# Optimization experiments

Measured on AMD Instinct MI355X. Metric: run time of the kernel, lower is better.

The kernel has to match this reference:

```python
import jax, jax.numpy as jnp
import numpy as np

N_NODES = 50000
N_EDGES = 800000
D_IN = 128
D_OUT = 128  # hidden_size == output_size == 128


def setup_inputs() -> dict:
    key = jax.random.key(0)
    k_x, k_src, k_dst, k_w1, k_w2 = jax.random.split(key, 5)
    x = jax.random.normal(k_x, (N_NODES, D_IN), dtype=jnp.float32)
    src = jax.random.randint(k_src, (N_EDGES,), 0, N_NODES)
    dst = jax.random.randint(k_dst, (N_EDGES,), 0, N_NODES)
    # SGConv fc weight (torch Linear layout: [out, in]) and bias
    w_conv = jax.random.normal(k_w1, (D_OUT, D_IN), dtype=jnp.float32) / np.sqrt(D_IN)
    b_conv = jnp.zeros((D_OUT,), dtype=jnp.float32)
    # trailing Linear(hidden_size=128 -> output_size=128)
    w_lin = jax.random.normal(k_w2, (D_OUT, D_OUT), dtype=jnp.float32) / np.sqrt(D_OUT)
    b_lin = jnp.zeros((D_OUT,), dtype=jnp.float32)
    return {"x": x, "src": src, "dst": dst,
            "w_conv": w_conv, "b_conv": b_conv,
            "w_lin": w_lin, "b_lin": b_lin}


def reference(x, src, dst, w_conv, b_conv, w_lin, b_lin):
    n = x.shape[0]
    # symmetric normalization by in-degree (DGL SGConv, k=1 hop)
    deg = jax.ops.segment_sum(jnp.ones_like(dst, dtype=x.dtype), dst, num_segments=n)
    norm = jax.lax.rsqrt(jnp.clip(deg, 1.0))[:, None]  # [N,1]
    h = x * norm                                        # D^{-1/2} X
    h = jax.ops.segment_sum(h[src], dst, num_segments=n)  # A (D^{-1/2} X), spmm via gather+scatter-add
    h = h * norm                                        # D^{-1/2} A D^{-1/2} X
    h = jnp.maximum(h @ w_conv.T + b_conv, 0.0)         # SGConv fc + relu
    return jnp.maximum(h @ w_lin.T + b_lin, 0.0)        # Linear + relu
```

## Files before the change

### kernel.cpp

```cpp
#include <hip/hip_runtime.h>

#define N_NODES 50000
#define N_EDGES 800000
#define D 128
#define ROWS 16
#define BCAP 255
#define LCAP 64
#define EDGE_BLOCKS 782
#define XCONV_BLOCKS 3125
#define NORM_BLOCKS 196
#define WSPLIT_BLOCKS 128
#define XB_OFF 200064
#define WS_NEEDED 13000064ull

typedef int   v4i __attribute__((ext_vector_type(4)));
typedef float v4f __attribute__((ext_vector_type(4)));


__device__ __forceinline__ unsigned short bf_rne(float v) {
    unsigned u = __float_as_uint(v);
    u += 0x7FFFu + ((u >> 16) & 1u);
    return (unsigned short)(u >> 16);
}
__device__ __forceinline__ float bf_up(unsigned short h) {
    return __uint_as_float((unsigned)h << 16);
}
__device__ __forceinline__ void split_pack(float a, float b, unsigned& hw, unsigned& lw) {
    unsigned short ha = bf_rne(a);
    unsigned short hb = bf_rne(b);
    unsigned short la = bf_rne(a - bf_up(ha));
    unsigned short lb = bf_rne(b - bf_up(hb));
    hw = (unsigned)ha | ((unsigned)hb << 16);
    lw = (unsigned)la | ((unsigned)lb << 16);
}
__device__ __forceinline__ unsigned pack2(float a, float b) {
    return (unsigned)bf_rne(a) | ((unsigned)bf_rne(b) << 16);
}

__global__ void scatter_kernel(const int4* __restrict__ src4,
                               const int4* __restrict__ dst4,
                               int* __restrict__ deg,
                               unsigned short* outSlots,
                               const float* __restrict__ x,
                               unsigned short* __restrict__ xb) {
    int b = blockIdx.x, t = threadIdx.x;
    if (b < EDGE_BLOCKS) {
        int e = b * 256 + t;
        if (e < N_EDGES / 4) {
            int4 s = src4[e];
            int4 d = dst4[e];
            int p;
            p = atomicAdd(&deg[d.x], 1); if (p < BCAP) outSlots[(size_t)d.x * 256 + p] = (unsigned short)s.x;
            p = atomicAdd(&deg[d.y], 1); if (p < BCAP) outSlots[(size_t)d.y * 256 + p] = (unsigned short)s.y;
            p = atomicAdd(&deg[d.z], 1); if (p < BCAP) outSlots[(size_t)d.z * 256 + p] = (unsigned short)s.z;
            p = atomicAdd(&deg[d.w], 1); if (p < BCAP) outSlots[(size_t)d.w * 256 + p] = (unsigned short)s.w;
        }
    } else {
        int i = (b - EDGE_BLOCKS) * 256 + t;
        if (i < N_NODES * D / 8) {
            float4 a = *(const float4*)(x + (size_t)8 * i);
            float4 c = *(const float4*)(x + (size_t)8 * i + 4);
            uint4 o;
            o.x = pack2(a.x, a.y);
            o.y = pack2(a.z, a.w);
            o.z = pack2(c.x, c.y);
            o.w = pack2(c.z, c.w);
            *(uint4*)(xb + (size_t)8 * i) = o;
        }
    }
}

__global__ void prep_kernel(const int* __restrict__ deg, float* __restrict__ normArr,
                            const float* __restrict__ w1, const float* __restrict__ w2,
                            unsigned short* __restrict__ whi1, unsigned short* __restrict__ wlo1,
                            unsigned short* __restrict__ whi2, unsigned short* __restrict__ wlo2) {
    int b = blockIdx.x, t = threadIdx.x;
    if (b < NORM_BLOCKS) {
        int n = b * 256 + t;
        if (n < N_NODES)
            normArr[n] = rsqrtf(fmaxf((float)deg[n], 1.0f));
    } else {
        int m = (b - NORM_BLOCKS) * 256 + t;
        int sel = m >> 14;
        int j = m & 16383;
        float v = sel ? w2[j] : w1[j];
        unsigned short h = bf_rne(v);
        unsigned short lo = bf_rne(v - bf_up(h));
        if (sel) { whi2[j] = h; wlo2[j] = lo; }
        else     { whi1[j] = h; wlo1[j] = lo; }
    }
}

#define MLP_BODY                                                               \
    int wv = t >> 6;                                                           \
    int cb = wv << 5;                                                          \
    int l15 = l & 15;                                                          \
    int kq = l >> 4;                                                           \
    const char* phiA = (const char*)&Ahi[l15][0];                              \
    const char* ploA = (const char*)&Alo[l15][0];                              \
    v4i ahi[4], alo[4];                                                        \
_Pragma("unroll")                                                              \
    for (int kt = 0; kt < 4; ++kt) {                                           \
        int off = ((((kt << 2) | kq) ^ l15) << 4);                             \
        ahi[kt] = *(const v4i*)(phiA + off);                                   \
        alo[kt] = *(const v4i*)(ploA + off);                                   \
    }                                                                          \
    __syncthreads();                                                           \
_Pragma("unroll")                                                              \
    for (int ct = 0; ct < 2; ++ct) {                                           \
        int c = cb + (ct << 4) + l15;                                          \
        float bv = b1[c];                                                      \
        v4f acc = {bv, bv, bv, bv};                                            \
        const unsigned short* wh = whi1 + c * D + (kq << 3);                   \
        const unsigned short* wl = wlo1 + c * D + (kq << 3);                   \
_Pragma("unroll")                                                              \
        for (int kt = 0; kt < 4; ++kt) {                                       \
            v4i bh = *(const v4i*)(wh + (kt << 5));                            \
            v4i bl = *(const v4i*)(wl + (kt << 5));                            \
            asm volatile("v_mfma_f32_16x16x32_bf16 %0, %1, %2, %0" : "+v"(acc) : "v"(ahi[kt]), "v"(bh)); \
            asm volatile("v_mfma_f32_16x16x32_bf16 %0, %1, %2, %0" : "+v"(acc) : "v"(alo[kt]), "v"(bh)); \
            asm volatile("v_mfma_f32_16x16x32_bf16 %0, %1, %2, %0" : "+v"(acc) : "v"(ahi[kt]), "v"(bl)); \
        }                                                                      \
        asm volatile("s_nop 7\n\ts_nop 7" : "+v"(acc));                        \
_Pragma("unroll")                                                              \
        for (int r = 0; r < 4; ++r) {                                          \
            float v = fmaxf(acc[r], 0.0f);                                     \
            unsigned short hv = bf_rne(v);                                     \
            unsigned short lv = bf_rne(v - bf_up(hv));                         \
            int ro = (kq << 2) + r;                                            \
            int byte = (2 * c) ^ ((ro & 15) << 4);                             \
            *(unsigned short*)((char*)&Ahi[ro][0] + byte) = hv;                \
            *(unsigned short*)((char*)&Alo[ro][0] + byte) = lv;                \
        }                                                                      \
    }                                                                          \
    __syncthreads();                                                           \
_Pragma("unroll")                                                              \
    for (int kt = 0; kt < 4; ++kt) {                                           \
        int off = ((((kt << 2) | kq) ^ l15) << 4);                             \
        ahi[kt] = *(const v4i*)(phiA + off);                                   \
        alo[kt] = *(const v4i*)(ploA + off);                                   \
    }                                                                          \
_Pragma("unroll")                                                              \
    for (int ct = 0; ct < 2; ++ct) {                                           \
        int c = cb + (ct << 4) + l15;                                          \
        float bv = b2[c];                                                      \
        v4f acc = {bv, bv, bv, bv};                                            \
        const unsigned short* wh = whi2 + c * D + (kq << 3);                   \
        const unsigned short* wl = wlo2 + c * D + (kq << 3);                   \
_Pragma("unroll")                                                              \
        for (int kt = 0; kt < 4; ++kt) {                                       \
            v4i bh = *(const v4i*)(wh + (kt << 5));                            \
            v4i bl = *(const v4i*)(wl + (kt << 5));                            \
            asm volatile("v_mfma_f32_16x16x32_bf16 %0, %1, %2, %0" : "+v"(acc) : "v"(ahi[kt]), "v"(bh)); \
            asm volatile("v_mfma_f32_16x16x32_bf16 %0, %1, %2, %0" : "+v"(acc) : "v"(alo[kt]), "v"(bh)); \
            asm volatile("v_mfma_f32_16x16x32_bf16 %0, %1, %2, %0" : "+v"(acc) : "v"(ahi[kt]), "v"(bl)); \
        }                                                                      \
        asm volatile("s_nop 7\n\ts_nop 7" : "+v"(acc));                        \
_Pragma("unroll")                                                              \
        for (int r = 0; r < 4; ++r) {                                          \
            int ro = row_base + (kq << 2) + r;                                 \
            if (ro < N_NODES)                                                  \
                io[(size_t)ro * D + c] = fmaxf(acc[r], 0.0f);                  \
        }                                                                      \
    }

__global__ __launch_bounds__(256) void fused_gather_mlp_bf16(
    const unsigned short* __restrict__ xb,
    const unsigned short* slotsIn,
    const float* __restrict__ normArr, const int* __restrict__ deg,
    float* io,
    const unsigned short* __restrict__ whi1, const unsigned short* __restrict__ wlo1,
    const float* __restrict__ b1,
    const unsigned short* __restrict__ whi2, const unsigned short* __restrict__ wlo2,
    const float* __restrict__ b2) {
    __shared__ __align__(16) unsigned short Ahi[ROWS][D];
    __shared__ __align__(16) unsigned short Alo[ROWS][D];
    __shared__ unsigned short colsL[ROWS][LCAP];
    __shared__ float ncolL[ROWS][LCAP];
    __shared__ int degL[ROWS];
    __shared__ int nextRow;
    int row_base = blockIdx.x * ROWS;
    int t = threadIdx.x;
    int tx = t & 31;
    int l = t & 63;

    if (t < ROWS) degL[t] = deg[row_base + t];
    if (t == ROWS) nextRow = 0;
    __syncthreads();

    for (int e2 = t; e2 < ROWS * LCAP; e2 += 256) {
        int r = e2 >> 6;
        int j = e2 & (LCAP - 1);
        if (j < degL[r]) {
            int s = slotsIn[(size_t)(row_base + r) * 256 + j];
            colsL[r][j] = (unsigned short)s;
            ncolL[r][j] = normArr[s];
        } else {
            colsL[r][j] = 0;
            ncolL[r][j] = 0.f;
        }
    }
    __syncthreads();

    for (;;) {
        int rr;
        if (tx == 0) rr = atomicAdd(&nextRow, 1);
        rr = __shfl(rr, l & 32);
        if (rr >= ROWS) break;
        int dr = degL[rr];
        float nr = rsqrtf(fmaxf((float)dr, 1.0f));
        float4 acc = make_float4(0.f, 0.f, 0.f, 0.f);
        int jend = min(dr, LCAP);
        for (int j = 0; j < jend; j += 8) {
            int s0 = colsL[rr][j + 0], s1 = colsL[rr][j + 1], s2 = colsL[rr][j + 2], s3 = colsL[rr][j + 3];
            int s4 = colsL[rr][j + 4], s5 = colsL[rr][j + 5], s6 = colsL[rr][j + 6], s7 = colsL[rr][j + 7];
            float n0 = ncolL[rr][j + 0], n1 = ncolL[rr][j + 1], n2 = ncolL[rr][j + 2], n3 = ncolL[rr][j + 3];
            float n4 = ncolL[rr][j + 4], n5 = ncolL[rr][j + 5], n6 = ncolL[rr][j + 6], n7 = ncolL[rr][j + 7];
            uint2 v0 = *(const uint2*)(xb + (size_t)s0 * D + 4 * tx);
            uint2 v1 = *(const uint2*)(xb + (size_t)s1 * D + 4 * tx);
            uint2 v2 = *(const uint2*)(xb + (size_t)s2 * D + 4 * tx);
            uint2 v3 = *(const uint2*)(xb + (size_t)s3 * D + 4 * tx);
            uint2 v4 = *(const uint2*)(xb + (size_t)s4 * D + 4 * tx);
            uint2 v5 = *(const uint2*)(xb + (size_t)s5 * D + 4 * tx);
            uint2 v6 = *(const uint2*)(xb + (size_t)s6 * D + 4 * tx);
            uint2 v7 = *(const uint2*)(xb + (size_t)s7 * D + 4 * tx);
            acc.x += __uint_as_float(v0.x << 16) * n0 + __uint_as_float(v1.x << 16) * n1
                   + __uint_as_float(v2.x << 16) * n2 + __uint_as_float(v3.x << 16) * n3
                   + __uint_as_float(v4.x << 16) * n4 + __uint_as_float(v5.x << 16) * n5
                   + __uint_as_float(v6.x << 16) * n6 + __uint_as_float(v7.x << 16) * n7;
            acc.y += __uint_as_float(v0.x & 0xffff0000u) * n0 + __uint_as_float(v1.x & 0xffff0000u) * n1
                   + __uint_as_float(v2.x & 0xffff0000u) * n2 + __uint_as_float(v3.x & 0xffff0000u) * n3
                   + __uint_as_float(v4.x & 0xffff0000u) * n4 + __uint_as_float(v5.x & 0xffff0000u) * n5
                   + __uint_as_float(v6.x & 0xffff0000u) * n6 + __uint_as_float(v7.x & 0xffff0000u) * n7;
            acc.z += __uint_as_float(v0.y << 16) * n0 + __uint_as_float(v1.y << 16) * n1
                   + __uint_as_float(v2.y << 16) * n2 + __uint_as_float(v3.y << 16) * n3
                   + __uint_as_float(v4.y << 16) * n4 + __uint_as_float(v5.y << 16) * n5
                   + __uint_as_float(v6.y << 16) * n6 + __uint_as_float(v7.y << 16) * n7;
            acc.w += __uint_as_float(v0.y & 0xffff0000u) * n0 + __uint_as_float(v1.y & 0xffff0000u) * n1
                   + __uint_as_float(v2.y & 0xffff0000u) * n2 + __uint_as_float(v3.y & 0xffff0000u) * n3
                   + __uint_as_float(v4.y & 0xffff0000u) * n4 + __uint_as_float(v5.y & 0xffff0000u) * n5
                   + __uint_as_float(v6.y & 0xffff0000u) * n6 + __uint_as_float(v7.y & 0xffff0000u) * n7;
        }
        if (dr > LCAP) {
            int je = min(dr, BCAP);
            for (int j = LCAP; j < je; ++j) {
                int s = slotsIn[(size_t)(row_base + rr) * 256 + j];
                float nv = normArr[s];
                uint2 v = *(const uint2*)(xb + (size_t)s * D + 4 * tx);
                acc.x += __uint_as_float(v.x << 16) * nv;
                acc.y += __uint_as_float(v.x & 0xffff0000u) * nv;
                acc.z += __uint_as_float(v.y << 16) * nv;
                acc.w += __uint_as_float(v.y & 0xffff0000u) * nv;
            }
        }
        acc.x *= nr; acc.y *= nr; acc.z *= nr; acc.w *= nr;
        unsigned hw0, lw0, hw1, lw1;
        split_pack(acc.x, acc.y, hw0, lw0);
        split_pack(acc.z, acc.w, hw1, lw1);
        int byte = (8 * tx) ^ ((rr & 15) << 4);
        *(uint2*)((char*)&Ahi[rr][0] + byte) = make_uint2(hw0, hw1);
        *(uint2*)((char*)&Alo[rr][0] + byte) = make_uint2(lw0, lw1);
    }
    __syncthreads();

    MLP_BODY
}

__global__ __launch_bounds__(256) void fused_gather_mlp_f32(
    const float* __restrict__ x,
    const unsigned short* slotsIn,
    const float* __restrict__ normArr, const int* __restrict__ deg,
    float* io,
    const unsigned short* __restrict__ whi1, const unsigned short* __restrict__ wlo1,
    const float* __restrict__ b1,
    const unsigned short* __restrict__ whi2, const unsigned short* __restrict__ wlo2,
    const float* __restrict__ b2) {
    __shared__ __align__(16) unsigned short Ahi[ROWS][D];
    __shared__ __align__(16) unsigned short Alo[ROWS][D];
    __shared__ unsigned short colsL[ROWS][LCAP];
    __shared__ float ncolL[ROWS][LCAP];
    __shared__ int degL[ROWS];
    __shared__ int nextRow;
    int row_base = blockIdx.x * ROWS;
    int t = threadIdx.x;
    int tx = t & 31;
    int l = t & 63;

    if (t < ROWS) degL[t] = deg[row_base + t];
    if (t == ROWS) nextRow = 0;
    __syncthreads();

    for (int e2 = t; e2 < ROWS * LCAP; e2 += 256) {
        int r = e2 >> 6;
        int j = e2 & (LCAP - 1);
        if (j < degL[r]) {
            int s = slotsIn[(size_t)(row_base + r) * 256 + j];
            colsL[r][j] = (unsigned short)s;
            ncolL[r][j] = normArr[s];
        } else {
            colsL[r][j] = 0;
            ncolL[r][j] = 0.f;
        }
    }
    __syncthreads();

    for (;;) {
        int rr;
        if (tx == 0) rr = atomicAdd(&nextRow, 1);
        rr = __shfl(rr, l & 32);
        if (rr >= ROWS) break;
        int dr = degL[rr];
        float nr = rsqrtf(fmaxf((float)dr, 1.0f));
        float4 acc = make_float4(0.f, 0.f, 0.f, 0.f);
        int jend = min(dr, LCAP);
        for (int j = 0; j < jend; j += 8) {
            int s0 = colsL[rr][j + 0], s1 = colsL[rr][j + 1], s2 = colsL[rr][j + 2], s3 = colsL[rr][j + 3];
            int s4 = colsL[rr][j + 4], s5 = colsL[rr][j + 5], s6 = colsL[rr][j + 6], s7 = colsL[rr][j + 7];
            float n0 = ncolL[rr][j + 0], n1 = ncolL[rr][j + 1], n2 = ncolL[rr][j + 2], n3 = ncolL[rr][j + 3];
            float n4 = ncolL[rr][j + 4], n5 = ncolL[rr][j + 5], n6 = ncolL[rr][j + 6], n7 = ncolL[rr][j + 7];
            float4 x0 = *(const float4*)(x + (size_t)s0 * D + 4 * tx);
            float4 x1 = *(const float4*)(x + (size_t)s1 * D + 4 * tx);
            float4 x2 = *(const float4*)(x + (size_t)s2 * D + 4 * tx);
            float4 x3 = *(const float4*)(x + (size_t)s3 * D + 4 * tx);
            float4 x4 = *(const float4*)(x + (size_t)s4 * D + 4 * tx);
            float4 x5 = *(const float4*)(x + (size_t)s5 * D + 4 * tx);
            float4 x6 = *(const float4*)(x + (size_t)s6 * D + 4 * tx);
            float4 x7 = *(const float4*)(x + (size_t)s7 * D + 4 * tx);
            acc.x += x0.x * n0 + x1.x * n1 + x2.x * n2 + x3.x * n3
                   + x4.x * n4 + x5.x * n5 + x6.x * n6 + x7.x * n7;
            acc.y += x0.y * n0 + x1.y * n1 + x2.y * n2 + x3.y * n3
                   + x4.y * n4 + x5.y * n5 + x6.y * n6 + x7.y * n7;
            acc.z += x0.z * n0 + x1.z * n1 + x2.z * n2 + x3.z * n3
                   + x4.z * n4 + x5.z * n5 + x6.z * n6 + x7.z * n7;
            acc.w += x0.w * n0 + x1.w * n1 + x2.w * n2 + x3.w * n3
                   + x4.w * n4 + x5.w * n5 + x6.w * n6 + x7.w * n7;
        }
        if (dr > LCAP) {
            int je = min(dr, BCAP);
            for (int j = LCAP; j < je; ++j) {
                int s = slotsIn[(size_t)(row_base + rr) * 256 + j];
                float nv = normArr[s];
                float4 xv = *(const float4*)(x + (size_t)s * D + 4 * tx);
                acc.x += xv.x * nv; acc.y += xv.y * nv;
                acc.z += xv.z * nv; acc.w += xv.w * nv;
            }
        }
        acc.x *= nr; acc.y *= nr; acc.z *= nr; acc.w *= nr;
        unsigned hw0, lw0, hw1, lw1;
        split_pack(acc.x, acc.y, hw0, lw0);
        split_pack(acc.z, acc.w, hw1, lw1);
        int byte = (8 * tx) ^ ((rr & 15) << 4);
        *(uint2*)((char*)&Ahi[rr][0] + byte) = make_uint2(hw0, hw1);
        *(uint2*)((char*)&Alo[rr][0] + byte) = make_uint2(lw0, lw1);
    }
    __syncthreads();

    MLP_BODY
}

extern "C" void kernel_launch(void* const* d_in, const int* in_sizes, int n_in,
                              void* d_out, int out_size, void* d_ws, size_t ws_size,
                              hipStream_t stream) {
    const float* x      = (const float*)d_in[0];
    const int*   src    = (const int*)d_in[1];
    int*         dstbuf = (int*)d_in[2];
    const float* w_conv = (const float*)d_in[3];
    const float* b_conv = (const float*)d_in[4];
    const float* w_lin  = (const float*)d_in[5];
    const float* b_lin  = (const float*)d_in[6];

    int* deg = (int*)d_ws;
    float* normArr = (float*)dstbuf;
    unsigned short* whi1 = (unsigned short*)((char*)dstbuf + 200000);
    unsigned short* wlo1 = (unsigned short*)((char*)dstbuf + 232768);
    unsigned short* whi2 = (unsigned short*)((char*)dstbuf + 265536);
    unsigned short* wlo2 = (unsigned short*)((char*)dstbuf + 298304);
    unsigned short* xb = (unsigned short*)((char*)d_ws + XB_OFF);
    const bool big = ws_size >= WS_NEEDED;

    hipMemsetAsync(deg, 0, (size_t)N_NODES * sizeof(int), stream);
    scatter_kernel<<<EDGE_BLOCKS + (big ? XCONV_BLOCKS : 0), 256, 0, stream>>>(
        (const int4*)src, (const int4*)dstbuf, deg, (unsigned short*)d_out, x, xb);
    prep_kernel<<<NORM_BLOCKS + WSPLIT_BLOCKS, 256, 0, stream>>>(
        deg, normArr, w_conv, w_lin, whi1, wlo1, whi2, wlo2);
    if (big) {
        fused_gather_mlp_bf16<<<N_NODES / ROWS, 256, 0, stream>>>(
            xb, (const unsigned short*)d_out, normArr, deg, (float*)d_out,
            whi1, wlo1, b_conv, whi2, wlo2, b_lin);
    } else {
        fused_gather_mlp_f32<<<N_NODES / ROWS, 256, 0, stream>>>(
            x, (const unsigned short*)d_out, normArr, deg, (float*)d_out,
            whi1, wlo1, b_conv, whi2, wlo2, b_lin);
    }
}
```

Before: 217.8 us.

## Fold weight split into scatter kernel and compute norms on the fly

The separate prep kernel is removed on the big-workspace path. The weight bf16 hi/lo split now runs as extra blocks of the scatter kernel, and the degree normalisation is recomputed from deg inside the gather kernel instead of being read from a precomputed norm array. The edge scatter also changes from four edges per thread (int4 loads) to one edge per thread with more blocks. This saves one kernel launch and its dependency barrier, at the cost of extra rsqrt work in the gather and more, smaller scatter blocks.

```diff
diff --git a/kernel.cpp b/kernel.cpp
--- a/kernel.cpp
+++ b/kernel.cpp
@@ -6,12 +6,13 @@
 #define ROWS 16
 #define BCAP 255
 #define LCAP 64
-#define EDGE_BLOCKS 782
+#define ESC_BLOCKS 3125
 #define XCONV_BLOCKS 3125
 #define NORM_BLOCKS 196
 #define WSPLIT_BLOCKS 128
 #define XB_OFF 200064
-#define WS_NEEDED 13000064ull
+#define WHI_OFF 13000064
+#define WS_NEEDED 13131136ull
 
 typedef int   v4i __attribute__((ext_vector_type(4)));
 typedef float v4f __attribute__((ext_vector_type(4)));
@@ -37,36 +38,37 @@
     return (unsigned)bf_rne(a) | ((unsigned)bf_rne(b) << 16);
 }
 
-__global__ void scatter_kernel(const int4* __restrict__ src4,
-                               const int4* __restrict__ dst4,
-                               int* __restrict__ deg,
-                               unsigned short* outSlots,
-                               const float* __restrict__ x,
-                               unsigned short* __restrict__ xb) {
+__global__ void scatter_kernel(const int* __restrict__ src, const int* __restrict__ dst,
+                               int* __restrict__ deg, unsigned short* outSlots,
+                               const float* __restrict__ x, unsigned short* __restrict__ xb,
+                               const float* __restrict__ w1, const float* __restrict__ w2,
+                               unsigned short* __restrict__ whi1, unsigned short* __restrict__ wlo1,
+                               unsigned short* __restrict__ whi2, unsigned short* __restrict__ wlo2) {
     int b = blockIdx.x, t = threadIdx.x;
-    if (b < EDGE_BLOCKS) {
+    if (b < ESC_BLOCKS) {
         int e = b * 256 + t;
-        if (e < N_EDGES / 4) {
-            int4 s = src4[e];
-            int4 d = dst4[e];
-            int p;
-            p = atomicAdd(&deg[d.x], 1); if (p < BCAP) outSlots[(size_t)d.x * 256 + p] = (unsigned short)s.x;
-            p = atomicAdd(&deg[d.y], 1); if (p < BCAP) outSlots[(size_t)d.y * 256 + p] = (unsigned short)s.y;
-            p = atomicAdd(&deg[d.z], 1); if (p < BCAP) outSlots[(size_t)d.z * 256 + p] = (unsigned short)s.z;
-            p = atomicAdd(&deg[d.w], 1); if (p < BCAP) outSlots[(size_t)d.w * 256 + p] = (unsigned short)s.w;
-        }
+        int s = src[e], d = dst[e];
+        int p = atomicAdd(&deg[d], 1);
+        if (p < BCAP) outSlots[(size_t)d * 256 + p] = (unsigned short)s;
+    } else if (b < ESC_BLOCKS + XCONV_BLOCKS) {
+        int i = (b - ESC_BLOCKS) * 256 + t;
+        float4 a = *(const float4*)(x + (size_t)8 * i);
+        float4 c = *(const float4*)(x + (size_t)8 * i + 4);
+        uint4 o;
+        o.x = pack2(a.x, a.y);
+        o.y = pack2(a.z, a.w);
+        o.z = pack2(c.x, c.y);
+        o.w = pack2(c.z, c.w);
+        *(uint4*)(xb + (size_t)8 * i) = o;
     } else {
-        int i = (b - EDGE_BLOCKS) * 256 + t;
-        if (i < N_NODES * D / 8) {
-            float4 a = *(const float4*)(x + (size_t)8 * i);
-            float4 c = *(const float4*)(x + (size_t)8 * i + 4);
-            uint4 o;
-            o.x = pack2(a.x, a.y);
-            o.y = pack2(a.z, a.w);
-            o.z = pack2(c.x, c.y);
-            o.w = pack2(c.z, c.w);
-            *(uint4*)(xb + (size_t)8 * i) = o;
-        }
+        int m = (b - ESC_BLOCKS - XCONV_BLOCKS) * 256 + t;
+        int sel = m >> 14;
+        int j = m & 16383;
+        float v = sel ? w2[j] : w1[j];
+        unsigned short h = bf_rne(v);
+        unsigned short lo = bf_rne(v - bf_up(h));
+        if (sel) { whi2[j] = h; wlo2[j] = lo; }
+        else     { whi1[j] = h; wlo1[j] = lo; }
     }
 }
 
@@ -167,7 +169,7 @@
 __global__ __launch_bounds__(256) void fused_gather_mlp_bf16(
     const unsigned short* __restrict__ xb,
     const unsigned short* slotsIn,
-    const float* __restrict__ normArr, const int* __restrict__ deg,
+    const int* __restrict__ deg,
     float* io,
     const unsigned short* __restrict__ whi1, const unsigned short* __restrict__ wlo1,
     const float* __restrict__ b1,
@@ -194,7 +196,7 @@
         if (j < degL[r]) {
             int s = slotsIn[(size_t)(row_base + r) * 256 + j];
             colsL[r][j] = (unsigned short)s;
-            ncolL[r][j] = normArr[s];
+            ncolL[r][j] = rsqrtf(fmaxf((float)deg[s], 1.0f));
         } else {
             colsL[r][j] = 0;
             ncolL[r][j] = 0.f;
@@ -245,7 +247,7 @@
             int je = min(dr, BCAP);
             for (int j = LCAP; j < je; ++j) {
                 int s = slotsIn[(size_t)(row_base + rr) * 256 + j];
-                float nv = normArr[s];
+                float nv = rsqrtf(fmaxf((float)deg[s], 1.0f));
                 uint2 v = *(const uint2*)(xb + (size_t)s * D + 4 * tx);
                 acc.x += __uint_as_float(v.x << 16) * nv;
                 acc.y += __uint_as_float(v.x & 0xffff0000u) * nv;
@@ -370,24 +372,32 @@
     const float* b_lin  = (const float*)d_in[6];
 
     int* deg = (int*)d_ws;
-    float* normArr = (float*)dstbuf;
-    unsigned short* whi1 = (unsigned short*)((char*)dstbuf + 200000);
-    unsigned short* wlo1 = (unsigned short*)((char*)dstbuf + 232768);
-    unsigned short* whi2 = (unsigned short*)((char*)dstbuf + 265536);
-    unsigned short* wlo2 = (unsigned short*)((char*)dstbuf + 298304);
     unsigned short* xb = (unsigned short*)((char*)d_ws + XB_OFF);
     const bool big = ws_size >= WS_NEEDED;
 
     hipMemsetAsync(deg, 0, (size_t)N_NODES * sizeof(int), stream);
-    scatter_kernel<<<EDGE_BLOCKS + (big ? XCONV_BLOCKS : 0), 256, 0, stream>>>(
-        (const int4*)src, (const int4*)dstbuf, deg, (unsigned short*)d_out, x, xb);
-    prep_kernel<<<NORM_BLOCKS + WSPLIT_BLOCKS, 256, 0, stream>>>(
-        deg, normArr, w_conv, w_lin, whi1, wlo1, whi2, wlo2);
     if (big) {
+        unsigned short* whi1 = (unsigned short*)((char*)d_ws + WHI_OFF);
+        unsigned short* wlo1 = (unsigned short*)((char*)d_ws + WHI_OFF + 32768);
+        unsigned short* whi2 = (unsigned short*)((char*)d_ws + WHI_OFF + 65536);
+        unsigned short* wlo2 = (unsigned short*)((char*)d_ws + WHI_OFF + 98304);
+        scatter_kernel<<<ESC_BLOCKS + XCONV_BLOCKS + WSPLIT_BLOCKS, 256, 0, stream>>>(
+            src, (const int*)dstbuf, deg, (unsigned short*)d_out, x, xb,
+            w_conv, w_lin, whi1, wlo1, whi2, wlo2);
         fused_gather_mlp_bf16<<<N_NODES / ROWS, 256, 0, stream>>>(
-            xb, (const unsigned short*)d_out, normArr, deg, (float*)d_out,
+            xb, (const unsigned short*)d_out, deg, (float*)d_out,
             whi1, wlo1, b_conv, whi2, wlo2, b_lin);
     } else {
+        float* normArr = (float*)dstbuf;
+        unsigned short* whi1 = (unsigned short*)((char*)dstbuf + 200000);
+        unsigned short* wlo1 = (unsigned short*)((char*)dstbuf + 232768);
+        unsigned short* whi2 = (unsigned short*)((char*)dstbuf + 265536);
+        unsigned short* wlo2 = (unsigned short*)((char*)dstbuf + 298304);
+        scatter_kernel<<<ESC_BLOCKS, 256, 0, stream>>>(
+            src, (const int*)dstbuf, deg, (unsigned short*)d_out, x, xb,
+            w_conv, w_lin, whi1, wlo1, whi2, wlo2);
+        prep_kernel<<<NORM_BLOCKS + WSPLIT_BLOCKS, 256, 0, stream>>>(
+            deg, normArr, w_conv, w_lin, whi1, wlo1, whi2, wlo2);
         fused_gather_mlp_f32<<<N_NODES / ROWS, 256, 0, stream>>>(
             x, (const unsigned short*)d_out, normArr, deg, (float*)d_out,
             whi1, wlo1, b_conv, whi2, wlo2, b_lin);
```

Result: faster. 204.6 us (-6.1%).
